# Kernel optimization log

Hardware: AMD Instinct MI355X
Metric: run time of the kernel (lower is better)

Reference implementation:

```python
import jax, jax.numpy as jnp
import numpy as np

K = 3
STRIDE = 1
PAD = 1
IN_CH = 64
OUT_CH = 128
ALPHA = 0.5  # scaling_factor
QMAX = 127.0  # 8-bit symmetric fake quant


def fake_quant(x):
    # per-tensor symmetric 8-bit fake quant with dynamic amax + STE
    amax = jnp.max(jnp.abs(jax.lax.stop_gradient(x)))
    s = jnp.where(amax > 0, amax / QMAX, 1.0)
    q = jnp.clip(jnp.round(x / s), -QMAX, QMAX) * s
    return x + jax.lax.stop_gradient(q - x)


def im2col(x, k, stride, pad):
    # x: (B, C, H, W) -> (B, C*k*k, h_out*w_out), torch.nn.functional.unfold order (C slowest, then kh, kw)
    B, C, H, W = x.shape
    h_out = (H + 2 * pad - k) // stride + 1
    w_out = (W + 2 * pad - k) // stride + 1
    xp = jnp.pad(x, ((0, 0), (0, 0), (pad, pad), (pad, pad)))
    patches = [xp[:, :, i:i + stride * h_out:stride, j:j + stride * w_out:stride]
               for i in range(k) for j in range(k)]  # fixed k*k loop
    cols = jnp.stack(patches, axis=2)  # (B, C, k*k, h_out, w_out)
    return cols.reshape(B, C * k * k, h_out * w_out), h_out, w_out


def setup_inputs() -> dict:
    key = jax.random.key(0)
    k1, k2 = jax.random.split(key)
    inp = jax.random.normal(k1, (16, IN_CH, 128, 128), dtype=jnp.float32)
    weight = jax.random.normal(k2, (OUT_CH, IN_CH, K, K), dtype=jnp.float32) * 0.05
    return {"input": inp, "weight": weight}


def reference(input, weight):
    bs = input.shape[0]
    ksize = IN_CH * K * K
    cols, h_out, w_out = im2col(input, K, STRIDE, PAD)  # (B, ksize, L)
    num_sliding = cols.shape[2]
    x = jnp.transpose(cols, (0, 2, 1)).reshape(-1, ksize)  # (B*L, ksize)
    w_flat = weight.reshape(OUT_CH, ksize)

    act_scale = jnp.max(jnp.abs(jax.lax.stop_gradient(x)), axis=0)       # (ksize,)
    weight_scale = jnp.max(jnp.abs(jax.lax.stop_gradient(w_flat)), axis=0)  # (ksize,)
    scale = act_scale ** ALPHA / weight_scale ** (1.0 - ALPHA)
    scale = jnp.where(scale == 0, 1.0, scale)

    x = fake_quant(x / scale)
    w_flat = fake_quant(w_flat * scale)

    out = jnp.einsum('nk,ok->no', x, w_flat)  # (B*L, OUT_CH)
    out = out.reshape(bs, num_sliding, OUT_CH)
    out = jnp.transpose(out, (0, 2, 1)).reshape(bs, OUT_CH, h_out, w_out)
    return out
```

## Files before the change

kernel.cpp:

```cpp
#include <hip/hip_runtime.h>

#define BATCH 16
#define CIN   64
#define HW    128
#define OC    128
#define KSIZE 576

typedef float float4v __attribute__((ext_vector_type(4)));
typedef int   int4v   __attribute__((ext_vector_type(4)));
typedef unsigned int uint;

#define WS_ACT   0
#define WS_WSC   576
#define WS_XMUL  1152
#define WS_SXSW  1728
#define WS_WQ_BYTE_OFF 8192

#define SWZ(x) ((((x) & 3) ^ (((x) >> 2) & 3)))
#define MAGIC 12582912.0f

__device__ __forceinline__ void async_cp16(const void* g, void* l) {
    __builtin_amdgcn_global_load_lds(
        (const __attribute__((address_space(1))) unsigned int*)g,
        (__attribute__((address_space(3))) unsigned int*)l, 16, 0, 0);
}

__global__ __launch_bounds__(256) void k_absmax(const float* __restrict__ in,
                                                const float* __restrict__ w,
                                                float* __restrict__ wsf) {
    const int tid = threadIdx.x, lane = tid & 63, wid = tid >> 6;
    if (blockIdx.x < 1024) {
        const int c = blockIdx.x >> 4, bs = blockIdx.x & 15;
        const float4v* p = (const float4v*)(in + (size_t)(bs * CIN + c) * (HW * HW));
        float m[9];
#pragma unroll
        for (int i = 0; i < 9; ++i) m[i] = 0.f;
        for (int e = tid; e < 4096; e += 256) {
            const int h = e >> 5, q = e & 31;
            const float4v v = p[e];
            const float a0 = fabsf(v[0]), a1 = fabsf(v[1]), a2 = fabsf(v[2]), a3 = fabsf(v[3]);
            const float m01 = fmaxf(a0, a1), m12 = fmaxf(a1, a2);
            const float mall = fmaxf(m01, fmaxf(a2, a3));
            const float mw0 = (q == 31) ? fmaxf(m01, a2) : mall;
            const float mw2 = (q == 0)  ? fmaxf(m12, a3) : mall;
            const bool h0 = (h <= 126), h2 = (h >= 1);
            m[0] = fmaxf(m[0], h0 ? mw0 : 0.f);
            m[1] = fmaxf(m[1], h0 ? mall : 0.f);
            m[2] = fmaxf(m[2], h0 ? mw2 : 0.f);
            m[3] = fmaxf(m[3], mw0);
            m[4] = fmaxf(m[4], mall);
            m[5] = fmaxf(m[5], mw2);
            m[6] = fmaxf(m[6], h2 ? mw0 : 0.f);
            m[7] = fmaxf(m[7], h2 ? mall : 0.f);
            m[8] = fmaxf(m[8], h2 ? mw2 : 0.f);
        }
#pragma unroll
        for (int i = 0; i < 9; ++i)
            for (int off = 32; off; off >>= 1)
                m[i] = fmaxf(m[i], __shfl_down(m[i], off));
        __shared__ float sred[4][9];
        if (lane == 0)
#pragma unroll
            for (int i = 0; i < 9; ++i) sred[wid][i] = m[i];
        __syncthreads();
        if (tid < 9) {
            float mm = fmaxf(fmaxf(sred[0][tid], sred[1][tid]),
                             fmaxf(sred[2][tid], sred[3][tid]));
            atomicMax((int*)(wsf + WS_ACT + c * 9 + tid), __float_as_int(mm));
        }
    } else {
        const int k = (blockIdx.x - 1024) * 4 + wid;
        float m = fmaxf(fabsf(w[lane * KSIZE + k]), fabsf(w[(lane + 64) * KSIZE + k]));
        for (int off = 32; off; off >>= 1) m = fmaxf(m, __shfl_down(m, off));
        if (lane == 0) wsf[WS_WSC + k] = m;
    }
}

__global__ __launch_bounds__(576) void k_scale_wq(const float* __restrict__ w,
                                                  float* __restrict__ wsf,
                                                  char* __restrict__ wq_s) {
    __shared__ float ls[576];
    __shared__ float redA[9], redB[9];
    const int t = threadIdx.x, o = blockIdx.x;
    const int lane = t & 63, wid = t >> 6;
    const float a = wsf[WS_ACT + t];
    const float wv = wsf[WS_WSC + t];
    float s = sqrtf(a) / sqrtf(wv);
    if (s == 0.f) s = 1.f;
    ls[t] = s;
    float v1 = a / s;
    float v2 = wv * s;
    for (int off = 32; off; off >>= 1) {
        v1 = fmaxf(v1, __shfl_down(v1, off));
        v2 = fmaxf(v2, __shfl_down(v2, off));
    }
    if (lane == 0) { redA[wid] = v1; redB[wid] = v2; }
    __syncthreads();
    float ax = redA[0], aw = redB[0];
#pragma unroll
    for (int i = 1; i < 9; ++i) { ax = fmaxf(ax, redA[i]); aw = fmaxf(aw, redB[i]); }
    const float sx = ax > 0.f ? ax / 127.f : 1.f;
    const float sw = aw > 0.f ? aw / 127.f : 1.f;
    const int r = t >> 6, c = t & 63, ko = c * 9 + r;
    float q = rintf((w[o * KSIZE + ko] * ls[ko]) / sw);
    q = fminf(127.f, fmaxf(-127.f, q));
    const int qi = (int)q;
    const int fc = c >> 4;
    wq_s[r * 8192 + o * 64 + ((fc ^ SWZ(o)) << 4) + (c & 15)] = (char)qi;
    if (o == 0) {
        wsf[WS_XMUL + t] = 1.0f / (ls[ko] * sx);
        if (t == 0) wsf[WS_SXSW] = sx * sw;
    }
}

__global__ __launch_bounds__(512, 4) void k_gemm(const float* __restrict__ in,
                                                 const char* __restrict__ wq_s,
                                                 const float* __restrict__ wsf,
                                                 float* __restrict__ out) {
    __shared__ int4v Bl4[4608];
    __shared__ float xml[576];
    char* Bl = (char*)Bl4;

    const int tid = threadIdx.x, lane = tid & 63, w = tid >> 6;
    const int xcd = blockIdx.x & 7, idx = blockIdx.x >> 3;
    const int oh = xcd * 16 + (idx & 15);
    const int b = idx >> 4;
    const int l15 = lane & 15, fsel = lane >> 4;
    const int ow0 = w * 16 + l15;

#pragma unroll
    for (int i = 0; i < 9; ++i)
        async_cp16(wq_s + i * 8192 + tid * 16, Bl + i * 8192 + tid * 16);
    if (tid < 144)
        ((float4v*)xml)[tid] = ((const float4v*)(wsf + WS_XMUL))[tid];
    __syncthreads();

    const float* pb = in + ((size_t)b * CIN + fsel * 16) * (HW * HW);

    int4v acc[8];
#pragma unroll
    for (int nt = 0; nt < 8; ++nt) acc[nt] = (int4v){0, 0, 0, 0};

#pragma unroll
    for (int r = 0; r < 9; ++r) {
        const int kh = r / 3, kw = r - 3 * kh;
        const int h = oh + kh - 1;
        if (h >= 0 && h < HW) {
            const int iw = ow0 + kw - 1;
            int iwc = iw;
            if (kw == 0) iwc = iw < 0 ? 0 : iw;
            if (kw == 2) iwc = iw > 127 ? 127 : iw;
            const float* p = pb + h * HW + iwc;
            float v[16];
#pragma unroll
            for (int j = 0; j < 16; ++j) v[j] = p[j * (HW * HW)];
            const float* xp = xml + r * 64 + (fsel << 4);
            float4v xq[4];
#pragma unroll
            for (int d = 0; d < 4; ++d) xq[d] = *(const float4v*)(xp + d * 4);
            uint pk[4];
#pragma unroll
            for (int d = 0; d < 4; ++d) {
                uint u[4];
#pragma unroll
                for (int j2 = 0; j2 < 4; ++j2)
                    u[j2] = __float_as_uint(fmaf(v[d * 4 + j2], xq[d][j2], MAGIC));
                const uint p01 = __builtin_amdgcn_perm(u[1], u[0], 0x0C0C0400u);
                const uint p23 = __builtin_amdgcn_perm(u[3], u[2], 0x0C0C0400u);
                pk[d] = __builtin_amdgcn_perm(p23, p01, 0x05040100u);
            }
            int4v af;
            if (kw != 1) {
                const uint msk = ((unsigned)iw < 128u) ? 0xFFFFFFFFu : 0u;
                af = (int4v){(int)(pk[0] & msk), (int)(pk[1] & msk),
                             (int)(pk[2] & msk), (int)(pk[3] & msk)};
            } else {
                af = (int4v){(int)pk[0], (int)pk[1], (int)pk[2], (int)pk[3]};
            }
#pragma unroll
            for (int nt = 0; nt < 8; ++nt) {
                const int br = nt * 16 + l15;
                const int4v bf = *(const int4v*)(Bl + r * 8192 + br * 64 +
                                                 ((fsel ^ SWZ(br)) << 4));
                acc[nt] = __builtin_amdgcn_mfma_i32_16x16x64_i8(af, bf, acc[nt], 0, 0, 0);
            }
        }
    }

    const float sxsw = wsf[WS_SXSW];
    const int owp = w * 16 + (fsel << 2);
#pragma unroll
    for (int nt = 0; nt < 8; ++nt) {
        const int o = nt * 16 + l15;
        float4v rv;
#pragma unroll
        for (int q = 0; q < 4; ++q) rv[q] = (float)acc[nt][q] * sxsw;
        *(float4v*)(out + ((size_t)(b * OC + o) * HW + oh) * HW + owp) = rv;
    }
}

extern "C" void kernel_launch(void* const* d_in, const int* in_sizes, int n_in,
                              void* d_out, int out_size, void* d_ws, size_t ws_size,
                              hipStream_t stream) {
    const float* in = (const float*)d_in[0];
    const float* wt = (const float*)d_in[1];
    float* out = (float*)d_out;
    float* wsf = (float*)d_ws;
    char* wq_s = (char*)d_ws + WS_WQ_BYTE_OFF;

    k_absmax<<<dim3(1024 + 144), dim3(256), 0, stream>>>(in, wt, wsf);
    k_scale_wq<<<dim3(128), dim3(576), 0, stream>>>(wt, wsf, wq_s);
    k_gemm<<<dim3(BATCH * HW), dim3(512), 0, stream>>>(in, wq_s, wsf, out);
}
```

Measured before the change: 224.3 us.

## Compute two output rows per block and two column tiles per wave

Restructures the GEMM tiling so each block handles two output rows and each wave computes two 16-column tiles with separate accumulators. The grid is halved, amortizing the per-block LDS staging of the quantized weights, and each B fragment read from LDS feeds two MFMAs. This doubles accumulator and activation registers per thread, which may reduce occupancy or cause spills, and leaves fewer blocks to hide memory latency.

```diff
diff --git a/kernel.cpp b/kernel.cpp
--- a/kernel.cpp
+++ b/kernel.cpp
@@ -123,10 +123,12 @@
 
     const int tid = threadIdx.x, lane = tid & 63, w = tid >> 6;
     const int xcd = blockIdx.x & 7, idx = blockIdx.x >> 3;
-    const int oh = xcd * 16 + (idx & 15);
-    const int b = idx >> 4;
+    const int ohp = idx & 7;
+    const int b = idx >> 3;
+    const int wh = w >> 2, wm = w & 3;
+    const int oh = xcd * 16 + ohp * 2 + wh;
     const int l15 = lane & 15, fsel = lane >> 4;
-    const int ow0 = w * 16 + l15;
+    const int ow0 = wm * 32 + l15;
 
 #pragma unroll
     for (int i = 0; i < 9; ++i)
@@ -137,65 +139,89 @@
 
     const float* pb = in + ((size_t)b * CIN + fsel * 16) * (HW * HW);
 
-    int4v acc[8];
-#pragma unroll
-    for (int nt = 0; nt < 8; ++nt) acc[nt] = (int4v){0, 0, 0, 0};
+    int4v acc0[8], acc1[8];
+#pragma unroll
+    for (int nt = 0; nt < 8; ++nt) {
+        acc0[nt] = (int4v){0, 0, 0, 0};
+        acc1[nt] = (int4v){0, 0, 0, 0};
+    }
 
 #pragma unroll
     for (int r = 0; r < 9; ++r) {
         const int kh = r / 3, kw = r - 3 * kh;
         const int h = oh + kh - 1;
         if (h >= 0 && h < HW) {
-            const int iw = ow0 + kw - 1;
-            int iwc = iw;
-            if (kw == 0) iwc = iw < 0 ? 0 : iw;
-            if (kw == 2) iwc = iw > 127 ? 127 : iw;
-            const float* p = pb + h * HW + iwc;
-            float v[16];
-#pragma unroll
-            for (int j = 0; j < 16; ++j) v[j] = p[j * (HW * HW)];
+            const int iw0 = ow0 + kw - 1;
+            const int iw1 = iw0 + 16;
+            int iwc0 = iw0, iwc1 = iw1;
+            if (kw == 0) iwc0 = iw0 < 0 ? 0 : iw0;
+            if (kw == 2) iwc1 = iw1 > 127 ? 127 : iw1;
+            const float* p0 = pb + h * HW + iwc0;
+            const float* p1 = pb + h * HW + iwc1;
+            float v0[16], v1[16];
+#pragma unroll
+            for (int j = 0; j < 16; ++j) {
+                v0[j] = p0[j * (HW * HW)];
+                v1[j] = p1[j * (HW * HW)];
+            }
             const float* xp = xml + r * 64 + (fsel << 4);
-            float4v xq[4];
-#pragma unroll
-            for (int d = 0; d < 4; ++d) xq[d] = *(const float4v*)(xp + d * 4);
-            uint pk[4];
+            uint pk0[4], pk1[4];
 #pragma unroll
             for (int d = 0; d < 4; ++d) {
-                uint u[4];
-#pragma unroll
-                for (int j2 = 0; j2 < 4; ++j2)
-                    u[j2] = __float_as_uint(fmaf(v[d * 4 + j2], xq[d][j2], MAGIC));
-                const uint p01 = __builtin_amdgcn_perm(u[1], u[0], 0x0C0C0400u);
-                const uint p23 = __builtin_amdgcn_perm(u[3], u[2], 0x0C0C0400u);
-                pk[d] = __builtin_amdgcn_perm(p23, p01, 0x05040100u);
-            }
-            int4v af;
-            if (kw != 1) {
-                const uint msk = ((unsigned)iw < 128u) ? 0xFFFFFFFFu : 0u;
-                af = (int4v){(int)(pk[0] & msk), (int)(pk[1] & msk),
-                             (int)(pk[2] & msk), (int)(pk[3] & msk)};
+                const float4v xq = *(const float4v*)(xp + d * 4);
+                uint u0[4], u1[4];
+#pragma unroll
+                for (int j2 = 0; j2 < 4; ++j2) {
+                    u0[j2] = __float_as_uint(fmaf(v0[d * 4 + j2], xq[j2], MAGIC));
+                    u1[j2] = __float_as_uint(fmaf(v1[d * 4 + j2], xq[j2], MAGIC));
+                }
+                const uint a01 = __builtin_amdgcn_perm(u0[1], u0[0], 0x0C0C0400u);
+                const uint a23 = __builtin_amdgcn_perm(u0[3], u0[2], 0x0C0C0400u);
+                pk0[d] = __builtin_amdgcn_perm(a23, a01, 0x05040100u);
+                const uint b01 = __builtin_amdgcn_perm(u1[1], u1[0], 0x0C0C0400u);
+                const uint b23 = __builtin_amdgcn_perm(u1[3], u1[2], 0x0C0C0400u);
+                pk1[d] = __builtin_amdgcn_perm(b23, b01, 0x05040100u);
+            }
+            int4v af0, af1;
+            if (kw == 0) {
+                const uint msk = ((unsigned)iw0 < 128u) ? 0xFFFFFFFFu : 0u;
+                af0 = (int4v){(int)(pk0[0] & msk), (int)(pk0[1] & msk),
+                              (int)(pk0[2] & msk), (int)(pk0[3] & msk)};
+                af1 = (int4v){(int)pk1[0], (int)pk1[1], (int)pk1[2], (int)pk1[3]};
+            } else if (kw == 2) {
+                const uint msk = ((unsigned)iw1 < 128u) ? 0xFFFFFFFFu : 0u;
+                af0 = (int4v){(int)pk0[0], (int)pk0[1], (int)pk0[2], (int)pk0[3]};
+                af1 = (int4v){(int)(pk1[0] & msk), (int)(pk1[1] & msk),
+                              (int)(pk1[2] & msk), (int)(pk1[3] & msk)};
             } else {
-                af = (int4v){(int)pk[0], (int)pk[1], (int)pk[2], (int)pk[3]};
+                af0 = (int4v){(int)pk0[0], (int)pk0[1], (int)pk0[2], (int)pk0[3]};
+                af1 = (int4v){(int)pk1[0], (int)pk1[1], (int)pk1[2], (int)pk1[3]};
             }
 #pragma unroll
             for (int nt = 0; nt < 8; ++nt) {
                 const int br = nt * 16 + l15;
                 const int4v bf = *(const int4v*)(Bl + r * 8192 + br * 64 +
                                                  ((fsel ^ SWZ(br)) << 4));
-                acc[nt] = __builtin_amdgcn_mfma_i32_16x16x64_i8(af, bf, acc[nt], 0, 0, 0);
+                acc0[nt] = __builtin_amdgcn_mfma_i32_16x16x64_i8(af0, bf, acc0[nt], 0, 0, 0);
+                acc1[nt] = __builtin_amdgcn_mfma_i32_16x16x64_i8(af1, bf, acc1[nt], 0, 0, 0);
             }
         }
     }
 
     const float sxsw = wsf[WS_SXSW];
-    const int owp = w * 16 + (fsel << 2);
+    const int owp = wm * 32 + (fsel << 2);
 #pragma unroll
     for (int nt = 0; nt < 8; ++nt) {
         const int o = nt * 16 + l15;
-        float4v rv;
-#pragma unroll
-        for (int q = 0; q < 4; ++q) rv[q] = (float)acc[nt][q] * sxsw;
-        *(float4v*)(out + ((size_t)(b * OC + o) * HW + oh) * HW + owp) = rv;
+        float4v rv0, rv1;
+#pragma unroll
+        for (int q = 0; q < 4; ++q) {
+            rv0[q] = (float)acc0[nt][q] * sxsw;
+            rv1[q] = (float)acc1[nt][q] * sxsw;
+        }
+        float* po = out + ((size_t)(b * OC + o) * HW + oh) * HW;
+        *(float4v*)(po + owp) = rv0;
+        *(float4v*)(po + owp + 16) = rv1;
     }
 }
 
@@ -210,5 +236,5 @@
 
     k_absmax<<<dim3(1024 + 144), dim3(256), 0, stream>>>(in, wt, wsf);
     k_scale_wq<<<dim3(128), dim3(576), 0, stream>>>(wt, wsf, wq_s);
-    k_gemm<<<dim3(BATCH * HW), dim3(512), 0, stream>>>(in, wq_s, wsf, out);
-}
+    k_gemm<<<dim3(BATCH * HW / 2), dim3(512), 0, stream>>>(in, wq_s, wsf, out);
+}
```

After: 222.3 us, median of 2. Within noise of the previous version (-0.9%).
